# Optimization experiments

Hardware: AMD Instinct MI355X
Metric: run time of the kernel (lower is better)

The kernel has to match this reference:

```python
import jax, jax.numpy as jnp
import numpy as np

N, F, H, E = 10000, 256, 256, 320000
TEMPERATURE = 1.0


def setup_inputs() -> dict:
    key = jax.random.key(0)
    k_x, k_ei, k_w1, k_b1, k_w2, k_b2 = jax.random.split(key, 6)
    x = jax.random.normal(k_x, (N, F), dtype=jnp.float32)
    edge_index = jax.random.randint(k_ei, (2, E), 0, N, dtype=jnp.int64)
    # PyTorch nn.Linear default init: U(-1/sqrt(fan_in), 1/sqrt(fan_in)), weight shape (out, in)
    lim1 = 1.0 / np.sqrt(2 * F)
    W1 = jax.random.uniform(k_w1, (H, 2 * F), dtype=jnp.float32, minval=-lim1, maxval=lim1)
    b1 = jax.random.uniform(k_b1, (H,), dtype=jnp.float32, minval=-lim1, maxval=lim1)
    lim2 = 1.0 / np.sqrt(H)
    W2 = jax.random.uniform(k_w2, (1, H), dtype=jnp.float32, minval=-lim2, maxval=lim2)
    b2 = jax.random.uniform(k_b2, (1,), dtype=jnp.float32, minval=-lim2, maxval=lim2)
    return {"x": x, "edge_index": edge_index, "W1": W1, "b1": b1, "W2": W2, "b2": b2}


def reference(x, edge_index, W1, b1, W2, b2):
    row, col = edge_index[0], edge_index[1]
    edge_feat = jnp.concatenate([x[row], x[col]], axis=-1)  # (E, 2F)
    h = jax.nn.relu(edge_feat @ W1.T + b1)                  # (E, H)
    logits = (h @ W2.T + b2).squeeze(-1)                    # (E,)
    m = jax.nn.sigmoid(logits / max(TEMPERATURE, 1e-6))
    return m
```

## Files before the change

kernel.cpp:

```cpp
#include <hip/hip_runtime.h>
#include <hip/hip_bf16.h>


typedef __attribute__((ext_vector_type(8))) short bf16x8;
typedef __attribute__((ext_vector_type(8))) unsigned short u16x8;
typedef __attribute__((ext_vector_type(4))) float f32x4;
typedef __attribute__((ext_vector_type(2))) float f32x2;

__device__ __forceinline__ unsigned short f2bf(float f) {
    __hip_bfloat16 h = __float2bfloat16(f);
    return *reinterpret_cast<unsigned short*>(&h);
}

__global__ __launch_bounds__(1024) void gemm_lds(const float* __restrict__ x,
                                                 const float* __restrict__ w1,
                                                 const float* __restrict__ b1,
                                                 unsigned char* __restrict__ uv,
                                                 int M) {
    __shared__ __align__(16) unsigned short Ws[256][264];

    const int t    = threadIdx.x;
    const int wave = t >> 6;
    const int lane = t & 63;
    const int lm   = lane & 15;
    const int lq   = lane >> 4;
    const int h    = blockIdx.x & 1;
    const int c    = blockIdx.x >> 1;

    {
        const int row = t >> 2;
        const int col = (t & 3) * 64;
        const float* wr = w1 + (size_t)row * 512 + h * 256 + col;
#pragma unroll
        for (int i = 0; i < 8; ++i) {
            float4 a = *(const float4*)(wr + i * 8);
            float4 b = *(const float4*)(wr + i * 8 + 4);
            u16x8 o = {f2bf(a.x), f2bf(a.y), f2bf(a.z), f2bf(a.w),
                       f2bf(b.x), f2bf(b.y), f2bf(b.z), f2bf(b.w)};
            *(u16x8*)&Ws[row][col + i * 8] = o;
        }
    }
    __syncthreads();

    for (int id = wave; id < 20; id += 16) {
        const int ti = id >> 2;
        const int q  = id & 3;
        const int m0 = (c * 5 + ti) * 16;
        const int r0 = q * 64;

        const int gr = m0 + lm;
        const float* xr = x + (size_t)(gr < M ? gr : (M - 1)) * 256 + lq * 8;

        f32x4 acc[4];
#pragma unroll
        for (int j = 0; j < 4; ++j) acc[j] = f32x4{0.f, 0.f, 0.f, 0.f};

#pragma unroll
        for (int kt = 0; kt < 8; ++kt) {
            float4 a = *(const float4*)(xr + kt * 32);
            float4 b = *(const float4*)(xr + kt * 32 + 4);
            bf16x8 xf;
            xf[0] = (short)f2bf(a.x); xf[1] = (short)f2bf(a.y);
            xf[2] = (short)f2bf(a.z); xf[3] = (short)f2bf(a.w);
            xf[4] = (short)f2bf(b.x); xf[5] = (short)f2bf(b.y);
            xf[6] = (short)f2bf(b.z); xf[7] = (short)f2bf(b.w);
#pragma unroll
            for (int j = 0; j < 4; ++j) {
                bf16x8 wf = *(const bf16x8*)&Ws[r0 + j * 16 + lm][kt * 32 + lq * 8];
                acc[j] = __builtin_amdgcn_mfma_f32_16x16x32_bf16(wf, xf, acc[j], 0, 0, 0);
            }
        }

        const int node = m0 + lm;
        if (node < M) {
            unsigned char* up = uv + (size_t)node * 512 + h * 256 + r0 + lq * 4;
#pragma unroll
            for (int j = 0; j < 4; ++j) {
                float4 bb = (h == 0)
                              ? *(const float4*)(b1 + r0 + j * 16 + lq * 4)
                              : float4{0.f, 0.f, 0.f, 0.f};
                unsigned int d = __builtin_amdgcn_cvt_pk_fp8_f32(
                    acc[j][0] + bb.x, acc[j][1] + bb.y, 0, false);
                d = __builtin_amdgcn_cvt_pk_fp8_f32(
                    acc[j][2] + bb.z, acc[j][3] + bb.w, d, true);
                *(unsigned int*)(up + j * 16) = d;
            }
        }
    }
}

__global__ __launch_bounds__(256) void edge_kernel(const unsigned char* __restrict__ uv,
                                                   const int* __restrict__ ei,
                                                   const float* __restrict__ w2,
                                                   const float* __restrict__ b2p,
                                                   float* __restrict__ out, int E) {
    const int lane = threadIdx.x & 63;
    const int g = lane >> 4;
    const int c = lane & 15;
    const int wid  = (blockIdx.x * blockDim.x + threadIdx.x) >> 6;
    const int nwav = (gridDim.x * blockDim.x) >> 6;
    const int nb   = E >> 2;

    float w2r[16];
#pragma unroll
    for (int i = 0; i < 4; ++i)
        *(float4*)&w2r[i * 4] = *(const float4*)(w2 + c * 16 + i * 4);
    const float b2 = b2p[0];

    for (int b = wid; b < nb; b += 2 * nwav) {
        const int bB = b + nwav;
        const bool has2 = bB < nb;

        const int e0 = b * 4 + g;
        const int r0 = ei[e0];
        const int c0 = ei[E + e0];
        const int e1 = has2 ? bB * 4 + g : e0;
        const int r1 = ei[e1];
        const int c1 = ei[E + e1];

        uint4 ua = *(const uint4*)(uv + (size_t)r0 * 512 + c * 16);
        uint4 va = *(const uint4*)(uv + (size_t)c0 * 512 + 256 + c * 16);
        uint4 ub = *(const uint4*)(uv + (size_t)r1 * 512 + c * 16);
        uint4 vb = *(const uint4*)(uv + (size_t)c1 * 512 + 256 + c * 16);

        unsigned int uw[4], vw[4];
        float p;

        *(uint4*)&uw[0] = ua; *(uint4*)&vw[0] = va;
        {
            float2 p2 = {0.f, 0.f};
#pragma unroll
            for (int w = 0; w < 4; ++w) {
                f32x2 u01 = __builtin_amdgcn_cvt_pk_f32_fp8(uw[w], false);
                f32x2 u23 = __builtin_amdgcn_cvt_pk_f32_fp8(uw[w], true);
                f32x2 v01 = __builtin_amdgcn_cvt_pk_f32_fp8(vw[w], false);
                f32x2 v23 = __builtin_amdgcn_cvt_pk_f32_fp8(vw[w], true);
                float s0 = fmaxf(u01.x + v01.x, 0.f);
                float s1 = fmaxf(u01.y + v01.y, 0.f);
                float s2 = fmaxf(u23.x + v23.x, 0.f);
                float s3 = fmaxf(u23.y + v23.y, 0.f);
                p2.x = fmaf(s0, w2r[4 * w + 0], p2.x);
                p2.y = fmaf(s1, w2r[4 * w + 1], p2.y);
                p2.x = fmaf(s2, w2r[4 * w + 2], p2.x);
                p2.y = fmaf(s3, w2r[4 * w + 3], p2.y);
            }
            p = p2.x + p2.y;
        }
#pragma unroll
        for (int off = 1; off < 16; off <<= 1)
            p += __shfl_xor(p, off, 64);
        if (c == 0) out[e0] = 1.f / (1.f + __expf(-(p + b2)));

        if (has2) {
            *(uint4*)&uw[0] = ub; *(uint4*)&vw[0] = vb;
            float2 p2 = {0.f, 0.f};
#pragma unroll
            for (int w = 0; w < 4; ++w) {
                f32x2 u01 = __builtin_amdgcn_cvt_pk_f32_fp8(uw[w], false);
                f32x2 u23 = __builtin_amdgcn_cvt_pk_f32_fp8(uw[w], true);
                f32x2 v01 = __builtin_amdgcn_cvt_pk_f32_fp8(vw[w], false);
                f32x2 v23 = __builtin_amdgcn_cvt_pk_f32_fp8(vw[w], true);
                float s0 = fmaxf(u01.x + v01.x, 0.f);
                float s1 = fmaxf(u01.y + v01.y, 0.f);
                float s2 = fmaxf(u23.x + v23.x, 0.f);
                float s3 = fmaxf(u23.y + v23.y, 0.f);
                p2.x = fmaf(s0, w2r[4 * w + 0], p2.x);
                p2.y = fmaf(s1, w2r[4 * w + 1], p2.y);
                p2.x = fmaf(s2, w2r[4 * w + 2], p2.x);
                p2.y = fmaf(s3, w2r[4 * w + 3], p2.y);
            }
            p = p2.x + p2.y;
#pragma unroll
            for (int off = 1; off < 16; off <<= 1)
                p += __shfl_xor(p, off, 64);
            if (c == 0) out[e1] = 1.f / (1.f + __expf(-(p + b2)));
        }
    }
}

extern "C" void kernel_launch(void* const* d_in, const int* in_sizes, int n_in,
                              void* d_out, int out_size, void* d_ws, size_t ws_size,
                              hipStream_t stream) {
    const float* x  = (const float*)d_in[0];
    const int*   ei = (const int*)d_in[1];
    const float* W1 = (const float*)d_in[2];
    const float* b1 = (const float*)d_in[3];
    const float* W2 = (const float*)d_in[4];
    const float* b2 = (const float*)d_in[5];
    float* out = (float*)d_out;

    const int N = in_sizes[0] / 256;
    const int E = in_sizes[1] / 2;

    unsigned char* uv = (unsigned char*)d_ws;

    const int ngrp = (N + 79) / 80;
    gemm_lds<<<ngrp * 2, 1024, 0, stream>>>(x, W1, b1, uv, N);

    edge_kernel<<<2048, 256, 0, stream>>>(uv, ei, W2, b2, out, E);
}
```

Measured before the change: 106.2 us.

## Give each GEMM wave three row tiles to reuse W fragments across MFMAs

New measurement: 108.7 us. +2.3%, slower.

```diff
diff --git a/kernel.cpp b/kernel.cpp
--- a/kernel.cpp
+++ b/kernel.cpp
@@ -12,11 +12,11 @@
     return *reinterpret_cast<unsigned short*>(&h);
 }
 
-__global__ __launch_bounds__(1024) void gemm_lds(const float* __restrict__ x,
-                                                 const float* __restrict__ w1,
-                                                 const float* __restrict__ b1,
-                                                 unsigned char* __restrict__ uv,
-                                                 int M) {
+__global__ __launch_bounds__(512) void gemm_lds(const float* __restrict__ x,
+                                                const float* __restrict__ w1,
+                                                const float* __restrict__ b1,
+                                                unsigned char* __restrict__ uv,
+                                                int M) {
     __shared__ __align__(16) unsigned short Ws[256][264];
 
     const int t    = threadIdx.x;
@@ -25,64 +25,99 @@
     const int lm   = lane & 15;
     const int lq   = lane >> 4;
     const int h    = blockIdx.x & 1;
-    const int c    = blockIdx.x >> 1;
+    const int g    = blockIdx.x >> 1;
 
     {
-        const int row = t >> 2;
-        const int col = (t & 3) * 64;
-        const float* wr = w1 + (size_t)row * 512 + h * 256 + col;
-#pragma unroll
-        for (int i = 0; i < 8; ++i) {
+        const int row  = t >> 1;
+        const int col0 = (t & 1) * 128;
+        const float* wr = w1 + (size_t)row * 512 + h * 256 + col0;
+#pragma unroll
+        for (int i = 0; i < 16; ++i) {
             float4 a = *(const float4*)(wr + i * 8);
             float4 b = *(const float4*)(wr + i * 8 + 4);
             u16x8 o = {f2bf(a.x), f2bf(a.y), f2bf(a.z), f2bf(a.w),
                        f2bf(b.x), f2bf(b.y), f2bf(b.z), f2bf(b.w)};
-            *(u16x8*)&Ws[row][col + i * 8] = o;
+            *(u16x8*)&Ws[row][col0 + i * 8] = o;
         }
     }
     __syncthreads();
 
-    for (int id = wave; id < 20; id += 16) {
-        const int ti = id >> 2;
-        const int q  = id & 3;
-        const int m0 = (c * 5 + ti) * 16;
-        const int r0 = q * 64;
-
-        const int gr = m0 + lm;
-        const float* xr = x + (size_t)(gr < M ? gr : (M - 1)) * 256 + lq * 8;
-
-        f32x4 acc[4];
-#pragma unroll
-        for (int j = 0; j < 4; ++j) acc[j] = f32x4{0.f, 0.f, 0.f, 0.f};
-
-#pragma unroll
-        for (int kt = 0; kt < 8; ++kt) {
-            float4 a = *(const float4*)(xr + kt * 32);
-            float4 b = *(const float4*)(xr + kt * 32 + 4);
-            bf16x8 xf;
-            xf[0] = (short)f2bf(a.x); xf[1] = (short)f2bf(a.y);
-            xf[2] = (short)f2bf(a.z); xf[3] = (short)f2bf(a.w);
-            xf[4] = (short)f2bf(b.x); xf[5] = (short)f2bf(b.y);
-            xf[6] = (short)f2bf(b.z); xf[7] = (short)f2bf(b.w);
-#pragma unroll
-            for (int j = 0; j < 4; ++j) {
-                bf16x8 wf = *(const bf16x8*)&Ws[r0 + j * 16 + lm][kt * 32 + lq * 8];
-                acc[j] = __builtin_amdgcn_mfma_f32_16x16x32_bf16(wf, xf, acc[j], 0, 0, 0);
-            }
-        }
-
-        const int node = m0 + lm;
+    const int tri = wave & 1;
+    const int q   = wave >> 1;
+    const int r0  = q * 64;
+    const int nb  = g * 96 + tri * 48;
+
+    const float* xr0;
+    const float* xr1;
+    const float* xr2;
+    {
+        int g0 = nb + 0 * 16 + lm;  g0 = g0 < M ? g0 : (M - 1);
+        int g1 = nb + 1 * 16 + lm;  g1 = g1 < M ? g1 : (M - 1);
+        int g2 = nb + 2 * 16 + lm;  g2 = g2 < M ? g2 : (M - 1);
+        xr0 = x + (size_t)g0 * 256 + lq * 8;
+        xr1 = x + (size_t)g1 * 256 + lq * 8;
+        xr2 = x + (size_t)g2 * 256 + lq * 8;
+    }
+
+    f32x4 acc[4][3];
+#pragma unroll
+    for (int j = 0; j < 4; ++j)
+#pragma unroll
+        for (int s = 0; s < 3; ++s) acc[j][s] = f32x4{0.f, 0.f, 0.f, 0.f};
+
+#pragma unroll 2
+    for (int kt = 0; kt < 8; ++kt) {
+        bf16x8 xf0, xf1, xf2;
+        {
+            float4 a = *(const float4*)(xr0 + kt * 32);
+            float4 b = *(const float4*)(xr0 + kt * 32 + 4);
+            xf0[0] = (short)f2bf(a.x); xf0[1] = (short)f2bf(a.y);
+            xf0[2] = (short)f2bf(a.z); xf0[3] = (short)f2bf(a.w);
+            xf0[4] = (short)f2bf(b.x); xf0[5] = (short)f2bf(b.y);
+            xf0[6] = (short)f2bf(b.z); xf0[7] = (short)f2bf(b.w);
+        }
+        {
+            float4 a = *(const float4*)(xr1 + kt * 32);
+            float4 b = *(const float4*)(xr1 + kt * 32 + 4);
+            xf1[0] = (short)f2bf(a.x); xf1[1] = (short)f2bf(a.y);
+            xf1[2] = (short)f2bf(a.z); xf1[3] = (short)f2bf(a.w);
+            xf1[4] = (short)f2bf(b.x); xf1[5] = (short)f2bf(b.y);
+            xf1[6] = (short)f2bf(b.z); xf1[7] = (short)f2bf(b.w);
+        }
+        {
+            float4 a = *(const float4*)(xr2 + kt * 32);
+            float4 b = *(const float4*)(xr2 + kt * 32 + 4);
+            xf2[0] = (short)f2bf(a.x); xf2[1] = (short)f2bf(a.y);
+            xf2[2] = (short)f2bf(a.z); xf2[3] = (short)f2bf(a.w);
+            xf2[4] = (short)f2bf(b.x); xf2[5] = (short)f2bf(b.y);
+            xf2[6] = (short)f2bf(b.z); xf2[7] = (short)f2bf(b.w);
+        }
+#pragma unroll
+        for (int j = 0; j < 4; ++j) {
+            bf16x8 wf = *(const bf16x8*)&Ws[r0 + j * 16 + lm][kt * 32 + lq * 8];
+            acc[j][0] = __builtin_amdgcn_mfma_f32_16x16x32_bf16(wf, xf0, acc[j][0], 0, 0, 0);
+            acc[j][1] = __builtin_amdgcn_mfma_f32_16x16x32_bf16(wf, xf1, acc[j][1], 0, 0, 0);
+            acc[j][2] = __builtin_amdgcn_mfma_f32_16x16x32_bf16(wf, xf2, acc[j][2], 0, 0, 0);
+        }
+    }
+
+    float4 bb[4];
+#pragma unroll
+    for (int j = 0; j < 4; ++j)
+        bb[j] = (h == 0) ? *(const float4*)(b1 + r0 + j * 16 + lq * 4)
+                         : float4{0.f, 0.f, 0.f, 0.f};
+
+#pragma unroll
+    for (int s = 0; s < 3; ++s) {
+        const int node = nb + s * 16 + lm;
         if (node < M) {
             unsigned char* up = uv + (size_t)node * 512 + h * 256 + r0 + lq * 4;
 #pragma unroll
             for (int j = 0; j < 4; ++j) {
-                float4 bb = (h == 0)
-                              ? *(const float4*)(b1 + r0 + j * 16 + lq * 4)
-                              : float4{0.f, 0.f, 0.f, 0.f};
                 unsigned int d = __builtin_amdgcn_cvt_pk_fp8_f32(
-                    acc[j][0] + bb.x, acc[j][1] + bb.y, 0, false);
+                    acc[j][s][0] + bb[j].x, acc[j][s][1] + bb[j].y, 0, false);
                 d = __builtin_amdgcn_cvt_pk_fp8_f32(
-                    acc[j][2] + bb.z, acc[j][3] + bb.w, d, true);
+                    acc[j][s][2] + bb[j].z, acc[j][s][3] + bb[j].w, d, true);
                 *(unsigned int*)(up + j * 16) = d;
             }
         }
@@ -194,8 +229,8 @@
 
     unsigned char* uv = (unsigned char*)d_ws;
 
-    const int ngrp = (N + 79) / 80;
-    gemm_lds<<<ngrp * 2, 1024, 0, stream>>>(x, W1, b1, uv, N);
+    const int ngrp = (N + 95) / 96;
+    gemm_lds<<<ngrp * 2, 512, 0, stream>>>(x, W1, b1, uv, N);
 
     edge_kernel<<<2048, 256, 0, stream>>>(uv, ei, W2, b2, out, E);
 }
```
